# Performance work log

Hardware: AMD Instinct MI355X
Metric: run time of the kernel (lower is better)

Reference implementation:

```python
import jax, jax.numpy as jnp
import numpy as np
import math

EMBED_DIM = 256
N_HEAD = 8
N_LEVELS = 4
N_POINTS = 4
HEAD_DIM = EMBED_DIM // N_HEAD
TOTAL_POINTS = N_HEAD * N_LEVELS * N_POINTS
SPATIAL = np.array([[100, 100], [50, 50], [25, 25], [13, 13]], dtype=np.int32)
BS = 2
LEN_Q = int(SPATIAL.prod(1).sum())  # 13294, encoder self-attention
LEN_V = LEN_Q


def setup_inputs() -> dict:
    key = jax.random.key(0)
    ks = jax.random.split(key, 12)
    s = 1.0 / math.sqrt(EMBED_DIM)
    inp = {
        'query': jax.random.normal(ks[0], (BS, LEN_Q, EMBED_DIM), jnp.float32),
        'reference_points': jax.random.uniform(ks[1], (BS, LEN_Q, N_LEVELS, 2), jnp.float32),
        'value': jax.random.normal(ks[2], (BS, LEN_V, EMBED_DIM), jnp.float32),
        'value_spatial_shapes': jnp.asarray(SPATIAL),
        'W_value': jax.random.normal(ks[3], (EMBED_DIM, EMBED_DIM), jnp.float32) * s,
        'b_value': jnp.zeros((EMBED_DIM,), jnp.float32),
        'W_off': jax.random.normal(ks[4], (TOTAL_POINTS * 2, EMBED_DIM), jnp.float32) * 0.01,
        'b_off': jax.random.normal(ks[5], (TOTAL_POINTS * 2,), jnp.float32),
        'W_attn': jax.random.normal(ks[6], (TOTAL_POINTS, EMBED_DIM), jnp.float32) * s,
        'b_attn': jnp.zeros((TOTAL_POINTS,), jnp.float32),
        'W_out': jax.random.normal(ks[7], (EMBED_DIM, EMBED_DIM), jnp.float32) * s,
        'b_out': jnp.zeros((EMBED_DIM,), jnp.float32),
        'zeta': jnp.ones((1, 1, 1, HEAD_DIM), jnp.float32),  # search_type='embed'
    }
    return inp


def _grid_sample_bilinear(img, gx, gy):
    """img: [B,H,W,c]; gx,gy: [B,Q,P] normalized to [-1,1].
    align_corners=False, padding_mode='zeros' (matches F.grid_sample)."""
    B, H, W, c = img.shape
    x = (gx + 1.0) * (0.5 * W) - 0.5
    y = (gy + 1.0) * (0.5 * H) - 0.5
    x0 = jnp.floor(x)
    y0 = jnp.floor(y)
    wx = (x - x0)[..., None]
    wy = (y - y0)[..., None]
    flat = img.reshape(B, H * W, c)

    def gather(xi, yi):
        m = (xi >= 0) & (xi < W) & (yi >= 0) & (yi < H)
        xi_c = jnp.clip(xi, 0, W - 1).astype(jnp.int32)
        yi_c = jnp.clip(yi, 0, H - 1).astype(jnp.int32)
        idx = (yi_c * W + xi_c).reshape(B, -1, 1)
        v = jnp.take_along_axis(flat, idx, axis=1).reshape(B, *xi.shape[1:], c)
        return v * m[..., None]

    v00 = gather(x0, y0)
    v01 = gather(x0 + 1, y0)
    v10 = gather(x0, y0 + 1)
    v11 = gather(x0 + 1, y0 + 1)
    return (v00 * (1 - wx) * (1 - wy) + v01 * wx * (1 - wy)
            + v10 * (1 - wx) * wy + v11 * wx * wy)


def reference(query, reference_points, value, value_spatial_shapes,
              W_value, b_value, W_off, b_off, W_attn, b_attn, W_out, b_out, zeta):
    bs, Len_q, _ = query.shape
    Len_v = value.shape[1]
    shapes = np.asarray(value_spatial_shapes)  # static ints

    # value projection + sparse gate (zeta, not pruned/searched)
    v = value @ W_value.T + b_value
    v = v.reshape(bs, Len_v, N_HEAD, HEAD_DIM) * zeta  # [bs,Lv,h,c]

    # sampling offsets and attention weights from query
    off = (query @ W_off.T + b_off).reshape(bs, Len_q, N_HEAD, N_LEVELS, N_POINTS, 2)
    attn = (query @ W_attn.T + b_attn).reshape(bs, Len_q, N_HEAD, N_LEVELS * N_POINTS)
    attn = jax.nn.softmax(attn, axis=-1).reshape(bs, Len_q, N_HEAD, N_LEVELS, N_POINTS)

    # reference_points last dim == 2 branch
    normalizer = jnp.asarray(shapes[:, ::-1], jnp.float32).reshape(1, 1, 1, N_LEVELS, 1, 2)  # (W,H)
    loc = reference_points.reshape(bs, Len_q, 1, N_LEVELS, 1, 2) + off / normalizer
    grids = 2.0 * loc - 1.0  # [bs,Lq,h,L,P,2]

    B = bs * N_HEAD
    out = jnp.zeros((B, Len_q, HEAD_DIM), jnp.float32)
    start = 0
    for lvl in range(N_LEVELS):
        h, w = int(shapes[lvl, 0]), int(shapes[lvl, 1])
        # [bs, h*w, nh, c] -> [bs*nh, h, w, c]
        v_l = v[:, start:start + h * w].transpose(0, 2, 1, 3).reshape(B, h, w, HEAD_DIM)
        g = grids[:, :, :, lvl].transpose(0, 2, 1, 3, 4).reshape(B, Len_q, N_POINTS, 2)
        samp = _grid_sample_bilinear(v_l, g[..., 0], g[..., 1])  # [B,Lq,P,c]
        a_l = attn[:, :, :, lvl].transpose(0, 2, 1, 3).reshape(B, Len_q, N_POINTS)
        out = out + jnp.einsum('bqpc,bqp->bqc', samp, a_l)
        start += h * w

    out = out.reshape(bs, N_HEAD, Len_q, HEAD_DIM).transpose(0, 2, 1, 3).reshape(bs, Len_q, EMBED_DIM)
    return out @ W_out.T + b_out
```

## Files before the change

kernel.cpp:

```cpp
#include <hip/hip_runtime.h>


#define LQ    13294
#define NTOK  26588
#define NE    6806528

typedef unsigned short ushort_t;
typedef __attribute__((ext_vector_type(8))) short short8;
typedef __attribute__((ext_vector_type(8))) unsigned short ushort8_t;
typedef __attribute__((ext_vector_type(4))) float float4_t;

__device__ __forceinline__ ushort_t f2b(float f) {
    unsigned int x = __float_as_uint(f);
    return (ushort_t)((x + 0x7fffu + ((x >> 16) & 1u)) >> 16);
}

__device__ __forceinline__ void gload16(const void* g, void* l) {
    __builtin_amdgcn_global_load_lds(
        (const __attribute__((address_space(1))) unsigned int*)g,
        (__attribute__((address_space(3))) unsigned int*)l, 16, 0, 0);
}

__device__ __forceinline__ void cvt_seg(const float* __restrict__ s,
                                        ushort_t* __restrict__ d,
                                        int n4, int gid, int stride) {
    const float4_t* s4 = (const float4_t*)s;
    for (int i = gid; i < n4; i += stride) {
        float4_t f = s4[i];
        ushort4 o;
        o.x = f2b(f.x); o.y = f2b(f.y); o.z = f2b(f.z); o.w = f2b(f.w);
        *(ushort4*)(d + (long)i * 4) = o;
    }
}

__global__ __launch_bounds__(256) void cvt_k(
    const float* q, const float* v, const float* Wv, const float* Wo,
    const float* Wa, const float* Wout,
    ushort_t* q_bf, ushort_t* v_bf, ushort_t* Wv_bf, ushort_t* WoWa_bf,
    ushort_t* Wout_bf)
{
    const int gid = blockIdx.x * 256 + threadIdx.x;
    const int stride = gridDim.x * 256;
    cvt_seg(q,    q_bf,            NE / 4,     gid, stride);
    cvt_seg(v,    v_bf,            NE / 4,     gid, stride);
    cvt_seg(Wv,   Wv_bf,           65536 / 4,  gid, stride);
    cvt_seg(Wo,   WoWa_bf,         65536 / 4,  gid, stride);
    cvt_seg(Wa,   WoWa_bf + 65536, 32768 / 4,  gid, stride);
    cvt_seg(Wout, Wout_bf,         65536 / 4,  gid, stride);
}

__device__ __forceinline__ void gemm_tile(
    const ushort_t* __restrict__ A,
    const ushort_t* __restrict__ W,
    int m0, int n0,
    ushort_t* As, ushort_t* Bs, float4_t acc[2][4])
{
    const int tid = threadIdx.x;
    const int w  = tid >> 6;
    const int ln = tid & 63;
    const int lr = ln >> 2;
    const int lc = (ln & 3) * 8;

    ushort_t* lA0 = As + (w * 2 + 0) * 512;
    ushort_t* lA1 = As + (w * 2 + 1) * 512;
    ushort_t* lB  = Bs + w * 512;
    const ushort_t* gA0 = A + (long)(m0 + w * 32 + lr) * 256 + lc;
    const ushort_t* gA1 = gA0 + 16 * 256;
    const ushort_t* gB  = W + (long)(n0 + w * 16 + lr) * 256 + lc;

    const int krow = (ln >> 4) * 8;
    const int fr   = ln & 15;

    for (int k0 = 0; k0 < 256; k0 += 32) {
        gload16(gA0 + k0, lA0);
        gload16(gA1 + k0, lA1);
        gload16(gB  + k0, lB);
        __syncthreads();

        short8 af[2], bfr[4];
        #pragma unroll
        for (int i = 0; i < 2; i++)
            af[i] = *(const short8*)(As + (w * 32 + i * 16 + fr) * 32 + krow);
        #pragma unroll
        for (int j = 0; j < 4; j++)
            bfr[j] = *(const short8*)(Bs + (j * 16 + fr) * 32 + krow);
        #pragma unroll
        for (int i = 0; i < 2; i++)
            #pragma unroll
            for (int j = 0; j < 4; j++)
                acc[i][j] = __builtin_amdgcn_mfma_f32_16x16x32_bf16(af[i], bfr[j], acc[i][j], 0, 0, 0);
        __syncthreads();
    }
}

__global__ __launch_bounds__(256) void gemm_fused_k(
    const ushort_t* __restrict__ q_bf, const ushort_t* __restrict__ v_bf,
    const ushort_t* __restrict__ Wv,   const ushort_t* __restrict__ WoWa,
    const float* __restrict__ b_value, const float* __restrict__ b_off,
    const float* __restrict__ b_attn,  const float* __restrict__ zeta,
    ushort_t* __restrict__ vproj, float* __restrict__ oa)
{
    __shared__ __align__(16) ushort_t As[128 * 32];
    __shared__ __align__(16) ushort_t Bs[64 * 32];

    const int z = blockIdx.z;
    const int bid = blockIdx.x;
    int x, y;
    if (z == 0) {
        if (bid >= 832) return;
        int id = (bid & 7) * 104 + (bid >> 3);
        x = id >> 2; y = id & 3;
    } else {
        int id = (bid & 7) * 156 + (bid >> 3);
        x = id / 6; y = id - x * 6;
    }
    const int m0 = x * 128;
    const int n0 = y * 64;

    float4_t acc[2][4] = {};
    gemm_tile(z ? q_bf : v_bf, z ? WoWa : Wv, m0, n0, As, Bs, acc);

    const int tid = threadIdx.x;
    const int w = tid >> 6, ln = tid & 63;
    const int col = ln & 15;
    const int rq  = (ln >> 4) * 4;
    #pragma unroll
    for (int j = 0; j < 4; j++) {
        int n = n0 + j * 16 + col;
        if (z == 0) {
            float bz = b_value[n];
            float zz = zeta[n & 31];
            long hbase = (long)(n >> 5) * NTOK;
            #pragma unroll
            for (int i = 0; i < 2; i++) {
                #pragma unroll
                for (int r = 0; r < 4; r++) {
                    int m = m0 + w * 32 + i * 16 + rq + r;
                    if (m < NTOK)
                        vproj[(hbase + m) * 32 + (n & 31)] = f2b((acc[i][j][r] + bz) * zz);
                }
            }
        } else {
            float bz = (n < 256) ? b_off[n] : b_attn[n - 256];
            #pragma unroll
            for (int i = 0; i < 2; i++) {
                #pragma unroll
                for (int r = 0; r < 4; r++) {
                    int m = m0 + w * 32 + i * 16 + rq + r;
                    if (m < NTOK) oa[(long)m * 384 + n] = acc[i][j][r] + bz;
                }
            }
        }
    }
}

__global__ __launch_bounds__(256) void gemm_out_k(
    const ushort_t* __restrict__ A,
    const ushort_t* __restrict__ W,
    const float* __restrict__ bias,
    float* __restrict__ C)
{
    __shared__ __align__(16) ushort_t As[128 * 32];
    __shared__ __align__(16) ushort_t Bs[64 * 32];

    const int bid = blockIdx.x;
    int id = (bid & 7) * 104 + (bid >> 3);
    const int m0 = (id >> 2) * 128;
    const int n0 = (id & 3) * 64;

    float4_t acc[2][4] = {};
    gemm_tile(A, W, m0, n0, As, Bs, acc);

    const int tid = threadIdx.x;
    const int w = tid >> 6, ln = tid & 63;
    const int col = ln & 15;
    const int rq  = (ln >> 4) * 4;
    #pragma unroll
    for (int j = 0; j < 4; j++) {
        int n = n0 + j * 16 + col;
        float bz = bias[n];
        #pragma unroll
        for (int i = 0; i < 2; i++) {
            #pragma unroll
            for (int r = 0; r < 4; r++) {
                int m = m0 + w * 32 + i * 16 + rq + r;
                if (m < NTOK) C[(long)m * 256 + n] = acc[i][j][r] + bz;
            }
        }
    }
}

__global__ __launch_bounds__(512) void sample_k(
    const float* __restrict__ refp,
    const ushort_t* __restrict__ v,
    const float* __restrict__ oa,
    ushort_t* __restrict__ outp)
{
    const int bid = blockIdx.x;
    const int h   = bid & 7;
    const int tid = threadIdx.x;
    const long t  = (long)(bid >> 3) * 8 + (tid >> 6);
    if (t >= NTOK) return;
    const int b  = (t >= LQ) ? 1 : 0;
    const int ln = tid & 63;
    const int p  = ln >> 2, g = ln & 3;
    const int lvl = p >> 2;
    const int Wi  = (lvl == 0) ? 100 : (lvl == 1) ? 50 : (lvl == 2) ? 25 : 13;
    const int st  = (lvl == 0) ? 0 : (lvl == 1) ? 10000 : (lvl == 2) ? 12500 : 13125;
    const float Wf = (float)Wi;

    float lg = oa[t * 384 + 256 + h * 16 + p];
    float smax = lg;
    #pragma unroll
    for (int d = 4; d < 64; d <<= 1) smax = fmaxf(smax, __shfl_xor(smax, d, 64));
    float ex = __expf(lg - smax);
    float sm = ex;
    #pragma unroll
    for (int d = 4; d < 64; d <<= 1) sm += __shfl_xor(sm, d, 64);
    const float a = ex / sm;

    float ox = oa[t * 384 + h * 32 + p * 2];
    float oy = oa[t * 384 + h * 32 + p * 2 + 1];
    float rx = refp[t * 8 + lvl * 2];
    float ry = refp[t * 8 + lvl * 2 + 1];

    float x = rx * Wf + ox - 0.5f;
    float y = ry * Wf + oy - 0.5f;
    float xf = floorf(x), yf = floorf(y);
    float wx = x - xf, wy = y - yf;
    int x0 = (int)xf, y0 = (int)yf;

    float mx0 = ((unsigned)x0       < (unsigned)Wi) ? (1.f - wx) : 0.f;
    float mx1 = ((unsigned)(x0 + 1) < (unsigned)Wi) ? wx         : 0.f;
    float my0 = ((unsigned)y0       < (unsigned)Wi) ? (1.f - wy) * a : 0.f;
    float my1 = ((unsigned)(y0 + 1) < (unsigned)Wi) ? wy * a         : 0.f;
    int x0c = min(max(x0, 0), Wi - 1);
    int x1c = min(max(x0 + 1, 0), Wi - 1);
    int y0c = min(max(y0, 0), Wi - 1);
    int y1c = min(max(y0 + 1, 0), Wi - 1);

    const int hb = h * NTOK + b * LQ + st;
    const int go = g * 16;
    const int r0 = hb + y0c * Wi, r1 = hb + y1c * Wi;
    const char* vb = (const char*)v;
    uint4 u00 = *(const uint4*)(vb + (((r0 + x0c) << 6) + go));
    uint4 u01 = *(const uint4*)(vb + (((r0 + x1c) << 6) + go));
    uint4 u10 = *(const uint4*)(vb + (((r1 + x0c) << 6) + go));
    uint4 u11 = *(const uint4*)(vb + (((r1 + x1c) << 6) + go));

    const float w00 = mx0 * my0, w01 = mx1 * my0;
    const float w10 = mx0 * my1, w11 = mx1 * my1;

    float4_t accA = {0.f, 0.f, 0.f, 0.f};
    float4_t accB = {0.f, 0.f, 0.f, 0.f};
    #define ACC8(U, WGT) \
        accA[0] += (WGT) * __uint_as_float((U).x << 16); \
        accA[1] += (WGT) * __uint_as_float((U).x & 0xffff0000u); \
        accA[2] += (WGT) * __uint_as_float((U).y << 16); \
        accA[3] += (WGT) * __uint_as_float((U).y & 0xffff0000u); \
        accB[0] += (WGT) * __uint_as_float((U).z << 16); \
        accB[1] += (WGT) * __uint_as_float((U).z & 0xffff0000u); \
        accB[2] += (WGT) * __uint_as_float((U).w << 16); \
        accB[3] += (WGT) * __uint_as_float((U).w & 0xffff0000u);
    ACC8(u00, w00)
    ACC8(u01, w01)
    ACC8(u10, w10)
    ACC8(u11, w11)
    #undef ACC8

    #pragma unroll
    for (int d = 32; d >= 4; d >>= 1) {
        #pragma unroll
        for (int c = 0; c < 4; c++) {
            accA[c] += __shfl_down(accA[c], d, 64);
            accB[c] += __shfl_down(accB[c], d, 64);
        }
    }

    if (p == 0) {
        ushort8_t o8;
        o8[0] = f2b(accA[0]); o8[1] = f2b(accA[1]);
        o8[2] = f2b(accA[2]); o8[3] = f2b(accA[3]);
        o8[4] = f2b(accB[0]); o8[5] = f2b(accB[1]);
        o8[6] = f2b(accB[2]); o8[7] = f2b(accB[3]);
        *(ushort8_t*)(outp + t * 256 + h * 32 + g * 8) = o8;
    }
}

extern "C" void kernel_launch(void* const* d_in, const int* in_sizes, int n_in,
                              void* d_out, int out_size, void* d_ws, size_t ws_size,
                              hipStream_t stream)
{
    char* ws = (char*)d_ws;
    ushort_t* vproj   = (ushort_t*)ws;
    float*    oa      = (float*)(ws + (long)NE * 2);
    ushort_t* q_bf    = (ushort_t*)(ws + (long)NE * 2 + (long)NTOK * 1536);
    ushort_t* outpre  = q_bf;
    ushort_t* v_bf    = q_bf + NE;
    ushort_t* Wv_bf   = v_bf + NE;
    ushort_t* WoWa_bf = Wv_bf + 65536;
    ushort_t* Wout_bf = WoWa_bf + 98304;

    cvt_k<<<1024, 256, 0, stream>>>(
        (const float*)d_in[0], (const float*)d_in[2], (const float*)d_in[4],
        (const float*)d_in[6], (const float*)d_in[8], (const float*)d_in[10],
        q_bf, v_bf, Wv_bf, WoWa_bf, Wout_bf);

    gemm_fused_k<<<dim3(1248, 1, 2), 256, 0, stream>>>(
        q_bf, v_bf, Wv_bf, WoWa_bf,
        (const float*)d_in[5], (const float*)d_in[7], (const float*)d_in[9],
        (const float*)d_in[12], vproj, oa);

    sample_k<<<8 * 3324, 512, 0, stream>>>(
        (const float*)d_in[1], vproj, oa, outpre);

    gemm_out_k<<<832, 256, 0, stream>>>(
        outpre, Wout_bf, (const float*)d_in[11], (float*)d_out);
}
```

Measured before the change: 243.5 us.

## Split sampling kernel into per-point setup phase and per-channel gather phase via LDS

The sampling kernel now runs in two phases. In the first, one thread per (token, point) computes the softmax weight, the bilinear corner offsets and the corner weights, and stores them in shared memory (padded to avoid bank conflicts). In the second, each thread handles four points for one channel group and accumulates them, which cuts the cross-lane shuffle reduction and removes the redundant per-channel-group setup math. Each block now covers 32 tokens instead of 8, so the grid shrinks, at the cost of a block barrier and some shared-memory traffic.

```diff
diff --git a/kernel.cpp b/kernel.cpp
--- a/kernel.cpp
+++ b/kernel.cpp
@@ -196,94 +196,122 @@
     const float* __restrict__ oa,
     ushort_t* __restrict__ outp)
 {
+    __shared__ __align__(16) int   p_ofs[576][4];
+    __shared__ __align__(16) float p_w[576][4];
     const int bid = blockIdx.x;
     const int h   = bid & 7;
+    const int tbase = (bid >> 3) * 32;
     const int tid = threadIdx.x;
-    const long t  = (long)(bid >> 3) * 8 + (tid >> 6);
-    if (t >= NTOK) return;
-    const int b  = (t >= LQ) ? 1 : 0;
-    const int ln = tid & 63;
-    const int p  = ln >> 2, g = ln & 3;
-    const int lvl = p >> 2;
-    const int Wi  = (lvl == 0) ? 100 : (lvl == 1) ? 50 : (lvl == 2) ? 25 : 13;
-    const int st  = (lvl == 0) ? 0 : (lvl == 1) ? 10000 : (lvl == 2) ? 12500 : 13125;
-    const float Wf = (float)Wi;
-
-    float lg = oa[t * 384 + 256 + h * 16 + p];
-    float smax = lg;
-    #pragma unroll
-    for (int d = 4; d < 64; d <<= 1) smax = fmaxf(smax, __shfl_xor(smax, d, 64));
-    float ex = __expf(lg - smax);
-    float sm = ex;
-    #pragma unroll
-    for (int d = 4; d < 64; d <<= 1) sm += __shfl_xor(sm, d, 64);
-    const float a = ex / sm;
-
-    float ox = oa[t * 384 + h * 32 + p * 2];
-    float oy = oa[t * 384 + h * 32 + p * 2 + 1];
-    float rx = refp[t * 8 + lvl * 2];
-    float ry = refp[t * 8 + lvl * 2 + 1];
-
-    float x = rx * Wf + ox - 0.5f;
-    float y = ry * Wf + oy - 0.5f;
-    float xf = floorf(x), yf = floorf(y);
-    float wx = x - xf, wy = y - yf;
-    int x0 = (int)xf, y0 = (int)yf;
-
-    float mx0 = ((unsigned)x0       < (unsigned)Wi) ? (1.f - wx) : 0.f;
-    float mx1 = ((unsigned)(x0 + 1) < (unsigned)Wi) ? wx         : 0.f;
-    float my0 = ((unsigned)y0       < (unsigned)Wi) ? (1.f - wy) * a : 0.f;
-    float my1 = ((unsigned)(y0 + 1) < (unsigned)Wi) ? wy * a         : 0.f;
-    int x0c = min(max(x0, 0), Wi - 1);
-    int x1c = min(max(x0 + 1, 0), Wi - 1);
-    int y0c = min(max(y0, 0), Wi - 1);
-    int y1c = min(max(y0 + 1, 0), Wi - 1);
-
-    const int hb = h * NTOK + b * LQ + st;
-    const int go = g * 16;
-    const int r0 = hb + y0c * Wi, r1 = hb + y1c * Wi;
-    const char* vb = (const char*)v;
-    uint4 u00 = *(const uint4*)(vb + (((r0 + x0c) << 6) + go));
-    uint4 u01 = *(const uint4*)(vb + (((r0 + x1c) << 6) + go));
-    uint4 u10 = *(const uint4*)(vb + (((r1 + x0c) << 6) + go));
-    uint4 u11 = *(const uint4*)(vb + (((r1 + x1c) << 6) + go));
-
-    const float w00 = mx0 * my0, w01 = mx1 * my0;
-    const float w10 = mx0 * my1, w11 = mx1 * my1;
-
-    float4_t accA = {0.f, 0.f, 0.f, 0.f};
-    float4_t accB = {0.f, 0.f, 0.f, 0.f};
-    #define ACC8(U, WGT) \
-        accA[0] += (WGT) * __uint_as_float((U).x << 16); \
-        accA[1] += (WGT) * __uint_as_float((U).x & 0xffff0000u); \
-        accA[2] += (WGT) * __uint_as_float((U).y << 16); \
-        accA[3] += (WGT) * __uint_as_float((U).y & 0xffff0000u); \
-        accB[0] += (WGT) * __uint_as_float((U).z << 16); \
-        accB[1] += (WGT) * __uint_as_float((U).z & 0xffff0000u); \
-        accB[2] += (WGT) * __uint_as_float((U).w << 16); \
-        accB[3] += (WGT) * __uint_as_float((U).w & 0xffff0000u);
-    ACC8(u00, w00)
-    ACC8(u01, w01)
-    ACC8(u10, w10)
-    ACC8(u11, w11)
-    #undef ACC8
-
-    #pragma unroll
-    for (int d = 32; d >= 4; d >>= 1) {
+
+    {
+        const int tok1 = tid >> 4, p = tid & 15;
+        const long t = tbase + tok1;
+        if (t < NTOK) {
+            const int lvl = p >> 2;
+            const int Wi  = (lvl == 0) ? 100 : (lvl == 1) ? 50 : (lvl == 2) ? 25 : 13;
+            const int st  = (lvl == 0) ? 0 : (lvl == 1) ? 10000 : (lvl == 2) ? 12500 : 13125;
+            const float Wf = (float)Wi;
+            const int b = (t >= LQ) ? 1 : 0;
+
+            float lg = oa[t * 384 + 256 + h * 16 + p];
+            float smax = lg;
+            #pragma unroll
+            for (int d = 1; d < 16; d <<= 1) smax = fmaxf(smax, __shfl_xor(smax, d, 64));
+            float ex = __expf(lg - smax);
+            float sm = ex;
+            #pragma unroll
+            for (int d = 1; d < 16; d <<= 1) sm += __shfl_xor(sm, d, 64);
+            const float a = ex / sm;
+
+            float ox = oa[t * 384 + h * 32 + p * 2];
+            float oy = oa[t * 384 + h * 32 + p * 2 + 1];
+            float rx = refp[t * 8 + lvl * 2];
+            float ry = refp[t * 8 + lvl * 2 + 1];
+
+            float x = rx * Wf + ox - 0.5f;
+            float y = ry * Wf + oy - 0.5f;
+            float xf = floorf(x), yf = floorf(y);
+            float wx = x - xf, wy = y - yf;
+            int x0 = (int)xf, y0 = (int)yf;
+
+            float mx0 = ((unsigned)x0       < (unsigned)Wi) ? (1.f - wx) : 0.f;
+            float mx1 = ((unsigned)(x0 + 1) < (unsigned)Wi) ? wx         : 0.f;
+            float my0 = ((unsigned)y0       < (unsigned)Wi) ? (1.f - wy) * a : 0.f;
+            float my1 = ((unsigned)(y0 + 1) < (unsigned)Wi) ? wy * a         : 0.f;
+            int x0c = min(max(x0, 0), Wi - 1);
+            int x1c = min(max(x0 + 1, 0), Wi - 1);
+            int y0c = min(max(y0, 0), Wi - 1);
+            int y1c = min(max(y0 + 1, 0), Wi - 1);
+
+            const int hb = h * NTOK + b * LQ + st;
+            const int r0 = hb + y0c * Wi, r1 = hb + y1c * Wi;
+            const int su = tid + (tid >> 3);
+            p_ofs[su][0] = (r0 + x0c) << 6;
+            p_ofs[su][1] = (r0 + x1c) << 6;
+            p_ofs[su][2] = (r1 + x0c) << 6;
+            p_ofs[su][3] = (r1 + x1c) << 6;
+            p_w[su][0] = mx0 * my0;
+            p_w[su][1] = mx1 * my0;
+            p_w[su][2] = mx0 * my1;
+            p_w[su][3] = mx1 * my1;
+        }
+    }
+    __syncthreads();
+
+    const int tok2 = tid >> 4, l16 = tid & 15, s = l16 >> 2, g = l16 & 3;
+    const long t = tbase + tok2;
+    if (t < NTOK) {
+        const char* vb = (const char*)v;
+        const unsigned go = g * 16;
+        const int ub = tok2 * 16 + s * 4;
+        float4_t accA = {0.f, 0.f, 0.f, 0.f};
+        float4_t accB = {0.f, 0.f, 0.f, 0.f};
+
+        #pragma unroll
+        for (int q = 0; q < 4; q++) {
+            const int u = ub + q;
+            const int su = u + (u >> 3);
+            int4     o  = *(const int4*)p_ofs[su];
+            float4_t w4 = *(const float4_t*)p_w[su];
+            uint4 u00 = *(const uint4*)(vb + (unsigned)(o.x + go));
+            uint4 u01 = *(const uint4*)(vb + (unsigned)(o.y + go));
+            uint4 u10 = *(const uint4*)(vb + (unsigned)(o.z + go));
+            uint4 u11 = *(const uint4*)(vb + (unsigned)(o.w + go));
+            #define ACC8(U, WGT) \
+                accA[0] += (WGT) * __uint_as_float((U).x << 16); \
+                accA[1] += (WGT) * __uint_as_float((U).x & 0xffff0000u); \
+                accA[2] += (WGT) * __uint_as_float((U).y << 16); \
+                accA[3] += (WGT) * __uint_as_float((U).y & 0xffff0000u); \
+                accB[0] += (WGT) * __uint_as_float((U).z << 16); \
+                accB[1] += (WGT) * __uint_as_float((U).z & 0xffff0000u); \
+                accB[2] += (WGT) * __uint_as_float((U).w << 16); \
+                accB[3] += (WGT) * __uint_as_float((U).w & 0xffff0000u);
+            ACC8(u00, w4.x)
+            ACC8(u01, w4.y)
+            ACC8(u10, w4.z)
+            ACC8(u11, w4.w)
+            #undef ACC8
+        }
+
         #pragma unroll
         for (int c = 0; c < 4; c++) {
-            accA[c] += __shfl_down(accA[c], d, 64);
-            accB[c] += __shfl_down(accB[c], d, 64);
-        }
-    }
-
-    if (p == 0) {
-        ushort8_t o8;
-        o8[0] = f2b(accA[0]); o8[1] = f2b(accA[1]);
-        o8[2] = f2b(accA[2]); o8[3] = f2b(accA[3]);
-        o8[4] = f2b(accB[0]); o8[5] = f2b(accB[1]);
-        o8[6] = f2b(accB[2]); o8[7] = f2b(accB[3]);
-        *(ushort8_t*)(outp + t * 256 + h * 32 + g * 8) = o8;
+            accA[c] += __shfl_down(accA[c], 8, 64);
+            accB[c] += __shfl_down(accB[c], 8, 64);
+        }
+        #pragma unroll
+        for (int c = 0; c < 4; c++) {
+            accA[c] += __shfl_down(accA[c], 4, 64);
+            accB[c] += __shfl_down(accB[c], 4, 64);
+        }
+
+        if (s == 0) {
+            ushort8_t o8;
+            o8[0] = f2b(accA[0]); o8[1] = f2b(accA[1]);
+            o8[2] = f2b(accA[2]); o8[3] = f2b(accA[3]);
+            o8[4] = f2b(accB[0]); o8[5] = f2b(accB[1]);
+            o8[6] = f2b(accB[2]); o8[7] = f2b(accB[3]);
+            *(ushort8_t*)(outp + t * 256 + h * 32 + g * 8) = o8;
+        }
     }
 }
 
@@ -311,7 +339,7 @@
         (const float*)d_in[5], (const float*)d_in[7], (const float*)d_in[9],
         (const float*)d_in[12], vproj, oa);
 
-    sample_k<<<8 * 3324, 512, 0, stream>>>(
+    sample_k<<<8 * 831, 512, 0, stream>>>(
         (const float*)d_in[1], vproj, oa, outpre);
 
     gemm_out_k<<<832, 256, 0, stream>>>(
```

Measured after the change: 222.9 us. 1.09x faster.
